# Performance work log

Hardware: AMD Instinct MI355X
Metric: run time of the kernel (lower is better)

## Reference

```python
import jax, jax.numpy as jnp
import numpy as np

B, S, E, H = 2, 2048, 1024, 16
D = E // H  # head_dim = 64


def setup_inputs() -> dict:
    key = jax.random.key(0)
    ks = jax.random.split(key, 9)
    s = 1.0 / np.sqrt(E)
    return {
        "x": jax.random.normal(ks[0], (B, S, E), dtype=jnp.float32),
        "Wq": jax.random.uniform(ks[1], (E, E), jnp.float32, -s, s),
        "bq": jax.random.uniform(ks[2], (E,), jnp.float32, -s, s),
        "Wk": jax.random.uniform(ks[3], (E, E), jnp.float32, -s, s),
        "bk": jax.random.uniform(ks[4], (E,), jnp.float32, -s, s),
        "Wv": jax.random.uniform(ks[5], (E, E), jnp.float32, -s, s),
        "bv": jax.random.uniform(ks[6], (E,), jnp.float32, -s, s),
        "Wo": jax.random.uniform(ks[7], (E, E), jnp.float32, -s, s),
        "bo": jax.random.uniform(ks[8], (E,), jnp.float32, -s, s),
    }


def reference(x, Wq, bq, Wk, bk, Wv, bv, Wo, bo):
    # QKV projections (torch Linear: x @ W.T + b), split into heads: [B,H,S,D]
    def proj(t, W, b):
        return (t @ W.T + b).reshape(B, S, H, D).transpose(0, 2, 1, 3)

    Q = proj(x, Wq, bq)
    K = proj(x, Wk, bk)
    V = proj(x, Wv, bv)
    # scores [B,H,S,S], scaled by sqrt(head_dim)
    score = jnp.einsum('bnqd,bnkd->bnqk', Q, K) / jnp.sqrt(jnp.float32(D))
    weights = jax.nn.softmax(score, axis=-1)
    out = jnp.einsum('bnql,bnld->bnqd', weights, V)  # [B,H,S,D]
    out = out.transpose(0, 2, 1, 3).reshape(B, S, E)
    return out @ Wo.T + bo
```

## Files before the change

### kernel.cpp

```cpp
#include <hip/hip_runtime.h>


#define B_ 2
#define S_ 2048
#define E_ 1024
#define H_ 16
#define D_ 64
#define M_ (B_ * S_)

typedef __attribute__((ext_vector_type(8))) _Float16 f16x8;
typedef __attribute__((ext_vector_type(4))) _Float16 f16x4;
typedef __attribute__((ext_vector_type(2))) _Float16 f16x2;
typedef __attribute__((ext_vector_type(4))) float f32x4;
typedef __attribute__((ext_vector_type(16))) float f32x16;
typedef __attribute__((ext_vector_type(8))) unsigned short u16x8;
typedef __attribute__((ext_vector_type(4))) unsigned int u32x4;

#define LOG2E  1.44269504f
#define CLOG2  4.32808512f

static __device__ __forceinline__ float bf16_to_f32(unsigned short u) {
    return __uint_as_float(((unsigned)u) << 16);
}
static __device__ __forceinline__ unsigned short f32_to_bf16(float f) {
    unsigned u = __float_as_uint(f);
    u += 0x7FFFu + ((u >> 16) & 1u);
    return (unsigned short)(u >> 16);
}
static __device__ __forceinline__ float load1_f32(const void* p, int i, bool isbf) {
    return isbf ? bf16_to_f32(((const unsigned short*)p)[i]) : ((const float*)p)[i];
}
static __device__ __forceinline__ void store1(void* p, size_t i, float v, bool isbf) {
    if (isbf) ((unsigned short*)p)[i] = f32_to_bf16(v);
    else      ((float*)p)[i] = v;
}
static __device__ __forceinline__ void gl2lds16(const void* g, void* l) {
    __builtin_amdgcn_global_load_lds((const __attribute__((address_space(1))) unsigned int*)g,
                                     (__attribute__((address_space(3))) unsigned int*)l, 16, 0, 0);
}
static __device__ __forceinline__ float rexp2(float x) {
    float r;
    asm("v_exp_f32 %0, %1" : "=v"(r) : "v"(x));
    return r;
}
static __device__ __forceinline__ unsigned pk2(float a, float b) {
    return __builtin_bit_cast(unsigned, __builtin_amdgcn_cvt_pkrtz(a, b));
}

__global__ __launch_bounds__(256) void convert_inputs(
    const void* __restrict__ x,  const void* __restrict__ wq,
    const void* __restrict__ wk, const void* __restrict__ wv,
    const void* __restrict__ wo,
    _Float16* __restrict__ x16, _Float16* __restrict__ w16,
    int* __restrict__ flag_out)
{
    __shared__ int sflag;
    const int tid = threadIdx.x;
    if (tid < 64) {
        const unsigned short hh = ((const unsigned short*)x)[2 * tid];
        const int e = (hh >> 7) & 0xFF;
        const bool sane = (e >= 0x60 && e <= 0x9F);
        const unsigned long long m = __ballot(sane);
        if (tid == 0) sflag = (__popcll(m) >= 48) ? 1 : 0;
    }
    __syncthreads();
    const bool isbf = sflag != 0;
    if (blockIdx.x == 0 && tid == 0) *flag_out = sflag;

    const size_t t = ((size_t)blockIdx.x * 256 + tid) * 8;
    const void* src; size_t off; _Float16* dst; float scale = 1.0f;
    if (t < (size_t)M_ * E_) { src = x; off = t; dst = x16 + t; }
    else {
        const size_t u = t - (size_t)M_ * E_;
        const int wsel = (int)(u >> 20);
        off = u & ((1u << 20) - 1);
        src = wsel == 0 ? wq : wsel == 1 ? wk : wsel == 2 ? wv : wo;
        dst = w16 + u;
        if (wsel == 0) scale = 0.125f * LOG2E;
    }
    f16x8 v;
    if (isbf) {
        u16x8 s = *(const u16x8*)((const unsigned short*)src + off);
        #pragma unroll
        for (int j = 0; j < 8; ++j) v[j] = (_Float16)(bf16_to_f32(s[j]) * scale);
    } else {
        const float* f = (const float*)src + off;
        f32x4 lo = *(const f32x4*)f;
        f32x4 hi = *(const f32x4*)(f + 4);
        #pragma unroll
        for (int j = 0; j < 4; ++j) {
            v[j]     = (_Float16)(lo[j] * scale);
            v[4 + j] = (_Float16)(hi[j] * scale);
        }
    }
    *(f16x8*)dst = v;
}

__global__ __launch_bounds__(256) void gemm_qkv(
    const _Float16* __restrict__ x16, const _Float16* __restrict__ w16,
    const void* __restrict__ bq, const void* __restrict__ bk, const void* __restrict__ bv,
    const int* __restrict__ flag,
    _Float16* __restrict__ Qb, _Float16* __restrict__ Kb, _Float16* __restrict__ VTb)
{
    __shared__ __align__(16) _Float16 As[128 * 64];
    __shared__ __align__(16) _Float16 Bs[128 * 64];
    const bool isbf = (*flag != 0);
    const int tid = threadIdx.x, wave = tid >> 6, lane = tid & 63;
    const int wm = wave >> 1, wn = wave & 1;
    const int qd = lane >> 4, ln = lane & 15;
    const int m0 = blockIdx.x * 128;
    const int by = blockIdx.y;
    const int wsel = by >> 3;
    const int n0 = (by & 7) * 128;
    const _Float16* W = w16 + ((size_t)wsel << 20);

    char* dX = (wsel == 2) ? (char*)Bs : (char*)As;
    char* dW = (wsel == 2) ? (char*)As : (char*)Bs;

    const _Float16* gx[4]; const _Float16* gw[4];
    char* lx[4]; char* lw[4];
    #pragma unroll
    for (int it = 0; it < 4; ++it) {
        const int seg = it * 256 + tid;
        const int row = seg >> 3, cg = seg & 7;
        const int scol = ((cg + row) & 7) * 8;
        gx[it] = x16 + (size_t)(m0 + row) * E_ + scol;
        gw[it] = W + (size_t)(n0 + row) * E_ + scol;
        lx[it] = dX + (size_t)(it * 256 + wave * 64) * 16;
        lw[it] = dW + (size_t)(it * 256 + wave * 64) * 16;
    }

    const int sw0 = ((qd - ln) & 7) * 8;
    const int sw1 = ((qd + 4 - ln) & 7) * 8;

    f32x4 acc[16] = {};

    for (int kt = 0; kt < E_; kt += 64) {
        __syncthreads();
        #pragma unroll
        for (int it = 0; it < 4; ++it) {
            gl2lds16(gx[it] + kt, lx[it]);
            gl2lds16(gw[it] + kt, lw[it]);
        }
        __syncthreads();
        #pragma unroll
        for (int kk = 0; kk < 2; ++kk) {
            const int sw = kk ? sw1 : sw0;
            f16x8 a[4], bfr[4];
            #pragma unroll
            for (int mt = 0; mt < 4; ++mt)
                a[mt] = *(const f16x8*)&As[((wm * 64 + mt * 16 + ln) << 6) + sw];
            #pragma unroll
            for (int nt = 0; nt < 4; ++nt)
                bfr[nt] = *(const f16x8*)&Bs[((wn * 64 + nt * 16 + ln) << 6) + sw];
            #pragma unroll
            for (int mt = 0; mt < 4; ++mt)
                #pragma unroll
                for (int nt = 0; nt < 4; ++nt)
                    acc[mt * 4 + nt] = __builtin_amdgcn_mfma_f32_16x16x32_f16(a[mt], bfr[nt], acc[mt * 4 + nt], 0, 0, 0);
        }
    }

    if (wsel != 2) {
        const void* bias = wsel == 0 ? bq : bk;
        const float bscale = (wsel == 0) ? 0.125f * LOG2E : 1.0f;
        _Float16* dst = wsel == 0 ? Qb : Kb;
        #pragma unroll
        for (int nt = 0; nt < 4; ++nt) {
            const int n = n0 + wn * 64 + nt * 16 + ln;
            const float bvv = load1_f32(bias, n, isbf) * bscale;
            const int h = n >> 6, d = n & 63;
            #pragma unroll
            for (int mt = 0; mt < 4; ++mt)
                #pragma unroll
                for (int r = 0; r < 4; ++r) {
                    const int m = m0 + wm * 64 + mt * 16 + qd * 4 + r;
                    const int b = m >> 11, s = m & (S_ - 1);
                    dst[((size_t)(b * H_ + h) * S_ + s) * D_ + d] =
                        (_Float16)(acc[mt * 4 + nt][r] + bvv);
                }
        }
    } else {
        #pragma unroll
        for (int mt = 0; mt < 4; ++mt)
            #pragma unroll
            for (int r = 0; r < 4; ++r) {
                const int e = n0 + wm * 64 + mt * 16 + qd * 4 + r;
                const float bvv = load1_f32(bv, e, isbf);
                const int h = e >> 6, d = e & 63;
                #pragma unroll
                for (int nt = 0; nt < 4; ++nt) {
                    const int sg = m0 + wn * 64 + nt * 16 + ln;
                    const int b = sg >> 11, s = sg & (S_ - 1);
                    VTb[((size_t)(b * H_ + h) * D_ + d) * S_ + s] =
                        (_Float16)(acc[mt * 4 + nt][r] + bvv);
                }
            }
    }
}

__global__ __launch_bounds__(256, 4) void attn(
    const _Float16* __restrict__ Q, const _Float16* __restrict__ K,
    const _Float16* __restrict__ VT, _Float16* __restrict__ AO)
{
    __shared__ __align__(16) char smem[32768];
    _Float16* Ksb = (_Float16*)smem;
    _Float16* Vsb = (_Float16*)(smem + 16384);

    const int tid = threadIdx.x, wave = tid >> 6, lane = tid & 63;
    const int rl = lane & 31, h = lane >> 5, r7 = rl & 7;
    const int qg = wave & 1, kh = wave >> 1;
    const int L = blockIdx.x;
    const int bh = ((L & 7) << 2) | ((L >> 3) & 3);
    const int qt = L >> 5;
    const int b = bh >> 4, hh = bh & (H_ - 1);

    const _Float16* Kbase = K + (size_t)bh * S_ * D_;
    const _Float16* Vbase = VT + (size_t)bh * D_ * S_;

    f16x8 qf[4];
    {
        const _Float16* qrow = Q + ((size_t)bh * S_ + qt * 64 + qg * 32 + rl) * D_ + h * 8;
        #pragma unroll
        for (int c = 0; c < 4; ++c) qf[c] = *(const f16x8*)(qrow + c * 16);
    }

    f16x8 ones;
    #pragma unroll
    for (int j = 0; j < 8; ++j) ones[j] = (_Float16)1.0f;

    const _Float16* kg[2]; const _Float16* vg[2]; int ldo[2];
    #pragma unroll
    for (int it = 0; it < 2; ++it) {
        const int seg = it * 256 + tid;
        const int row = seg >> 3, cg = seg & 7;
        const int scol = ((cg ^ (row & 7)) << 3);
        kg[it] = Kbase + (size_t)row * D_ + scol;
        vg[it] = Vbase + (size_t)row * S_ + scol;
        ldo[it] = (it * 256 + wave * 64) * 16;
    }

    int koff[4];
    #pragma unroll
    for (int c = 0; c < 4; ++c)
        koff[c] = ((kh * 32 + rl) << 7) + ((((c << 1) | h) ^ r7) << 4);
    const int vrow0 = rl << 7, vrow1 = (32 + rl) << 7;
    const int hb = h << 3;

    f32x16 o0 = {}, o1 = {}, li = {};

    #pragma unroll
    for (int it = 0; it < 2; ++it) {
        gl2lds16(kg[it], (char*)Ksb + ldo[it]);
        gl2lds16(vg[it], (char*)Vsb + ldo[it]);
    }
    __syncthreads();

    for (int kt = 0; kt < S_; kt += 64) {
        const int p = (kt >> 6) & 1;
        if (kt + 64 < S_) {
            const int np = p ^ 1;
            #pragma unroll
            for (int it = 0; it < 2; ++it) {
                gl2lds16(kg[it] + (size_t)(kt + 64) * D_, (char*)Ksb + np * 8192 + ldo[it]);
                gl2lds16(vg[it] + (kt + 64),              (char*)Vsb + np * 8192 + ldo[it]);
            }
        }

        const char* kb = (const char*)Ksb + p * 8192;
        const char* vb = (const char*)Vsb + p * 8192;

        f16x8 af[4];
        #pragma unroll
        for (int c = 0; c < 4; ++c) af[c] = *(const f16x8*)(kb + koff[c]);

        f32x16 sc = {};
        __builtin_amdgcn_s_setprio(1);
        #pragma unroll
        for (int c = 0; c < 4; ++c)
            sc = __builtin_amdgcn_mfma_f32_32x32x16_f16(af[c], qf[c], sc, 0, 0, 0);
        __builtin_amdgcn_s_setprio(0);

        float e[16];
        #pragma unroll
        for (int i = 0; i < 16; ++i) e[i] = rexp2(sc[i] - CLOG2);

        #pragma unroll
        for (int ks = 0; ks < 2; ++ks) {
            const int oo = 8 * ks;
            const f16x8 pf = __builtin_bit_cast(f16x8, (u32x4){
                pk2(e[oo + 0], e[oo + 1]), pk2(e[oo + 2], e[oo + 3]),
                pk2(e[oo + 4], e[oo + 5]), pk2(e[oo + 6], e[oo + 7])});

            const int cA = ((((kh << 2) | (ks << 1)) ^ r7) << 4) + hb;
            const int cB = ((((kh << 2) | (ks << 1) | 1) ^ r7) << 4) + hb;
            const f16x4 a0 = *(const f16x4*)(vb + vrow0 + cA);
            const f16x4 b0 = *(const f16x4*)(vb + vrow0 + cB);
            const f16x4 a1 = *(const f16x4*)(vb + vrow1 + cA);
            const f16x4 b1 = *(const f16x4*)(vb + vrow1 + cB);
            const f16x8 v0 = __builtin_shufflevector(a0, b0, 0, 1, 2, 3, 4, 5, 6, 7);
            const f16x8 v1 = __builtin_shufflevector(a1, b1, 0, 1, 2, 3, 4, 5, 6, 7);

            __builtin_amdgcn_s_setprio(1);
            o0 = __builtin_amdgcn_mfma_f32_32x32x16_f16(pf, v0, o0, 0, 0, 0);
            o1 = __builtin_amdgcn_mfma_f32_32x32x16_f16(pf, v1, o1, 0, 0, 0);
            li = __builtin_amdgcn_mfma_f32_32x32x16_f16(pf, ones, li, 0, 0, 0);
            __builtin_amdgcn_s_setprio(0);
        }

        __syncthreads();
    }

    float* red = (float*)smem;
    const int rbase = qg * 64 + lane;
    if (kh) {
        #pragma unroll
        for (int i = 0; i < 16; ++i) {
            red[i * 128 + rbase]        = o0[i];
            red[(16 + i) * 128 + rbase] = o1[i];
            red[(32 + i) * 128 + rbase] = li[i];
        }
    }
    __syncthreads();
    if (!kh) {
        #pragma unroll
        for (int i = 0; i < 16; ++i) {
            const float t0 = o0[i] + red[i * 128 + rbase];
            const float t1 = o1[i] + red[(16 + i) * 128 + rbase];
            const float tl = li[i] + red[(32 + i) * 128 + rbase];
            const float inv = 1.0f / tl;
            const int q = qt * 64 + qg * 32 + 4 * h + (i & 3) + 8 * (i >> 2);
            _Float16* dst = AO + ((size_t)b * S_ + q) * E_ + hh * D_;
            dst[rl]      = (_Float16)(t0 * inv);
            dst[32 + rl] = (_Float16)(t1 * inv);
        }
    }
}

__global__ __launch_bounds__(256) void gemm_out(
    const _Float16* __restrict__ A, const _Float16* __restrict__ W,
    const void* __restrict__ bias, const int* __restrict__ flag, void* __restrict__ out)
{
    __shared__ __align__(16) _Float16 As[128 * 64];
    __shared__ __align__(16) _Float16 Bs[128 * 64];
    const bool isbf = (*flag != 0);
    const int tid = threadIdx.x, wave = tid >> 6, lane = tid & 63;
    const int wm = wave >> 1, wn = wave & 1;
    const int qd = lane >> 4, ln = lane & 15;
    const int m0 = blockIdx.x * 128;
    const int n0 = blockIdx.y * 128;

    const _Float16* ga[4]; const _Float16* gb[4];
    char* la[4]; char* lb[4];
    #pragma unroll
    for (int it = 0; it < 4; ++it) {
        const int seg = it * 256 + tid;
        const int row = seg >> 3, cg = seg & 7;
        const int scol = ((cg + row) & 7) * 8;
        ga[it] = A + (size_t)(m0 + row) * E_ + scol;
        gb[it] = W + (size_t)(n0 + row) * E_ + scol;
        la[it] = (char*)As + (size_t)(it * 256 + wave * 64) * 16;
        lb[it] = (char*)Bs + (size_t)(it * 256 + wave * 64) * 16;
    }
    const int sw0 = ((qd - ln) & 7) * 8;
    const int sw1 = ((qd + 4 - ln) & 7) * 8;

    f32x4 acc[16] = {};

    for (int kt = 0; kt < E_; kt += 64) {
        __syncthreads();
        #pragma unroll
        for (int it = 0; it < 4; ++it) {
            gl2lds16(ga[it] + kt, la[it]);
            gl2lds16(gb[it] + kt, lb[it]);
        }
        __syncthreads();
        #pragma unroll
        for (int kk = 0; kk < 2; ++kk) {
            const int sw = kk ? sw1 : sw0;
            f16x8 a[4], bfr[4];
            #pragma unroll
            for (int mt = 0; mt < 4; ++mt)
                a[mt] = *(const f16x8*)&As[((wm * 64 + mt * 16 + ln) << 6) + sw];
            #pragma unroll
            for (int nt = 0; nt < 4; ++nt)
                bfr[nt] = *(const f16x8*)&Bs[((wn * 64 + nt * 16 + ln) << 6) + sw];
            #pragma unroll
            for (int mt = 0; mt < 4; ++mt)
                #pragma unroll
                for (int nt = 0; nt < 4; ++nt)
                    acc[mt * 4 + nt] = __builtin_amdgcn_mfma_f32_16x16x32_f16(a[mt], bfr[nt], acc[mt * 4 + nt], 0, 0, 0);
        }
    }

    #pragma unroll
    for (int nt = 0; nt < 4; ++nt) {
        const int n = n0 + wn * 64 + nt * 16 + ln;
        const float bvv = load1_f32(bias, n, isbf);
        #pragma unroll
        for (int mt = 0; mt < 4; ++mt)
            #pragma unroll
            for (int r = 0; r < 4; ++r) {
                const int m = m0 + wm * 64 + mt * 16 + qd * 4 + r;
                store1(out, (size_t)m * E_ + n, acc[mt * 4 + nt][r] + bvv, isbf);
            }
    }
}

extern "C" void kernel_launch(void* const* d_in, const int* in_sizes, int n_in,
                              void* d_out, int out_size, void* d_ws, size_t ws_size,
                              hipStream_t stream) {
    const void* x  = d_in[0];
    const void* Wq = d_in[1];
    const void* bq = d_in[2];
    const void* Wk = d_in[3];
    const void* bk = d_in[4];
    const void* Wv = d_in[5];
    const void* bv = d_in[6];
    const void* Wo = d_in[7];
    const void* bo = d_in[8];

    int* flag = (int*)d_ws;
    _Float16* x16 = (_Float16*)((char*)d_ws + 1024);
    _Float16* w16 = x16 + (size_t)M_ * E_;
    _Float16* Qb  = w16 + 4u * (size_t)E_ * E_;
    _Float16* Kb  = Qb + (size_t)M_ * E_;
    _Float16* VTb = Kb + (size_t)M_ * E_;
    _Float16* AO  = x16;

    convert_inputs<<<4096, 256, 0, stream>>>(x, Wq, Wk, Wv, Wo, x16, w16, flag);
    gemm_qkv<<<dim3(32, 24), 256, 0, stream>>>(x16, w16, bq, bk, bv, flag, Qb, Kb, VTb);
    attn<<<1024, 256, 0, stream>>>(Qb, Kb, VTb, AO);
    gemm_out<<<dim3(32, 8), 256, 0, stream>>>(AO, w16 + 3u * (size_t)E_ * E_, bo, flag, d_out);
}
```

Baseline: 207.2 us.

## Stage K/V tiles through registers into padded LDS instead of direct global-to-LDS loads

Result: no change. 204.1 us (-1.5%).

```diff
diff --git a/kernel.cpp b/kernel.cpp
--- a/kernel.cpp
+++ b/kernel.cpp
@@ -18,6 +18,11 @@
 
 #define LOG2E  1.44269504f
 #define CLOG2  4.32808512f
+
+#define KROW 144
+#define KBUF 9216
+#define VBASE 18432
+#define SMEMSZ 36864
 
 static __device__ __forceinline__ float bf16_to_f32(unsigned short u) {
     return __uint_as_float(((unsigned)u) << 16);
@@ -203,12 +208,10 @@
     const _Float16* __restrict__ Q, const _Float16* __restrict__ K,
     const _Float16* __restrict__ VT, _Float16* __restrict__ AO)
 {
-    __shared__ __align__(16) char smem[32768];
-    _Float16* Ksb = (_Float16*)smem;
-    _Float16* Vsb = (_Float16*)(smem + 16384);
+    __shared__ __align__(16) char smem[SMEMSZ];
 
     const int tid = threadIdx.x, wave = tid >> 6, lane = tid & 63;
-    const int rl = lane & 31, h = lane >> 5, r7 = rl & 7;
+    const int rl = lane & 31, h = lane >> 5;
     const int qg = wave & 1, kh = wave >> 1;
     const int L = blockIdx.x;
     const int bh = ((L & 7) << 2) | ((L >> 3) & 3);
@@ -229,46 +232,52 @@
     #pragma unroll
     for (int j = 0; j < 8; ++j) ones[j] = (_Float16)1.0f;
 
-    const _Float16* kg[2]; const _Float16* vg[2]; int ldo[2];
+    const _Float16* kg[2]; const _Float16* vg[2]; int sw[2];
     #pragma unroll
     for (int it = 0; it < 2; ++it) {
         const int seg = it * 256 + tid;
-        const int row = seg >> 3, cg = seg & 7;
-        const int scol = ((cg ^ (row & 7)) << 3);
-        kg[it] = Kbase + (size_t)row * D_ + scol;
-        vg[it] = Vbase + (size_t)row * S_ + scol;
-        ldo[it] = (it * 256 + wave * 64) * 16;
+        const int row = seg >> 3, c = seg & 7;
+        kg[it] = Kbase + (size_t)row * D_ + c * 8;
+        vg[it] = Vbase + (size_t)row * S_ + c * 8;
+        sw[it] = row * KROW + c * 16;
     }
 
     int koff[4];
     #pragma unroll
     for (int c = 0; c < 4; ++c)
-        koff[c] = ((kh * 32 + rl) << 7) + ((((c << 1) | h) ^ r7) << 4);
-    const int vrow0 = rl << 7, vrow1 = (32 + rl) << 7;
-    const int hb = h << 3;
+        koff[c] = (kh * 32 + rl) * KROW + (((c << 1) | h) << 4);
+    const int vrow0 = rl * KROW, vrow1 = (32 + rl) * KROW;
+    const int vka = kh * 64 + h * 8;
 
     f32x16 o0 = {}, o1 = {}, li = {};
 
-    #pragma unroll
-    for (int it = 0; it < 2; ++it) {
-        gl2lds16(kg[it], (char*)Ksb + ldo[it]);
-        gl2lds16(vg[it], (char*)Vsb + ldo[it]);
+    {
+        f16x8 kr[2], vr[2];
+        #pragma unroll
+        for (int it = 0; it < 2; ++it) { kr[it] = *(const f16x8*)kg[it]; vr[it] = *(const f16x8*)vg[it]; }
+        #pragma unroll
+        for (int it = 0; it < 2; ++it) {
+            *(f16x8*)(smem + sw[it])         = kr[it];
+            *(f16x8*)(smem + VBASE + sw[it]) = vr[it];
+        }
     }
     __syncthreads();
 
     for (int kt = 0; kt < S_; kt += 64) {
         const int p = (kt >> 6) & 1;
-        if (kt + 64 < S_) {
-            const int np = p ^ 1;
+        const bool more = (kt + 64) < S_;
+
+        f16x8 kr[2], vr[2];
+        if (more) {
             #pragma unroll
             for (int it = 0; it < 2; ++it) {
-                gl2lds16(kg[it] + (size_t)(kt + 64) * D_, (char*)Ksb + np * 8192 + ldo[it]);
-                gl2lds16(vg[it] + (kt + 64),              (char*)Vsb + np * 8192 + ldo[it]);
+                kr[it] = *(const f16x8*)(kg[it] + (size_t)(kt + 64) * D_);
+                vr[it] = *(const f16x8*)(vg[it] + (kt + 64));
             }
         }
 
-        const char* kb = (const char*)Ksb + p * 8192;
-        const char* vb = (const char*)Vsb + p * 8192;
+        const char* kb = smem + p * KBUF;
+        const char* vb = smem + VBASE + p * KBUF;
 
         f16x8 af[4];
         #pragma unroll
@@ -292,12 +301,11 @@
                 pk2(e[oo + 0], e[oo + 1]), pk2(e[oo + 2], e[oo + 3]),
                 pk2(e[oo + 4], e[oo + 5]), pk2(e[oo + 6], e[oo + 7])});
 
-            const int cA = ((((kh << 2) | (ks << 1)) ^ r7) << 4) + hb;
-            const int cB = ((((kh << 2) | (ks << 1) | 1) ^ r7) << 4) + hb;
+            const int cA = vka + ks * 32;
             const f16x4 a0 = *(const f16x4*)(vb + vrow0 + cA);
-            const f16x4 b0 = *(const f16x4*)(vb + vrow0 + cB);
+            const f16x4 b0 = *(const f16x4*)(vb + vrow0 + cA + 16);
             const f16x4 a1 = *(const f16x4*)(vb + vrow1 + cA);
-            const f16x4 b1 = *(const f16x4*)(vb + vrow1 + cB);
+            const f16x4 b1 = *(const f16x4*)(vb + vrow1 + cA + 16);
             const f16x8 v0 = __builtin_shufflevector(a0, b0, 0, 1, 2, 3, 4, 5, 6, 7);
             const f16x8 v1 = __builtin_shufflevector(a1, b1, 0, 1, 2, 3, 4, 5, 6, 7);
 
@@ -308,6 +316,13 @@
             __builtin_amdgcn_s_setprio(0);
         }
 
+        if (more) {
+            #pragma unroll
+            for (int it = 0; it < 2; ++it) {
+                *(f16x8*)(smem + (p ^ 1) * KBUF + sw[it])         = kr[it];
+                *(f16x8*)(smem + VBASE + (p ^ 1) * KBUF + sw[it]) = vr[it];
+            }
+        }
         __syncthreads();
     }
 
```
